# Kernel optimization log

Measured on AMD Instinct MI355X. Metric: run time of the kernel, lower is better.

The kernel has to match this reference:

```python
import jax, jax.numpy as jnp
import numpy as np

KERNEL_MUL = 2.0
KERNEL_NUM = 5
FIX_SIGMA = None

B = 256  # batch size of each domain
D = 256  # feature dim


def setup_inputs() -> dict:
    key = jax.random.key(0)
    k1, k2 = jax.random.split(key)
    source = jax.random.normal(k1, (B, D), dtype=jnp.float32)
    target = jax.random.normal(k2, (B, D), dtype=jnp.float32)
    return {"source": source, "target": target}


def reference(source, target):
    b = source.shape[0]
    total = jnp.concatenate([source, target], axis=0)  # (2B, D)
    n = total.shape[0]
    # pairwise diffs, then CUMULATIVE squared distance along feature axis
    # (faithful to the original's torch.cumsum quirk) -> (2B, 2B, D)
    diff = total[:, None, :] - total[None, :, :]
    l2_cum = jnp.cumsum(diff * diff, axis=2)
    if FIX_SIGMA:
        bandwidth = jnp.asarray(FIX_SIGMA, dtype=l2_cum.dtype)
    else:
        bandwidth = jnp.sum(l2_cum) / (n * n - n)
    bandwidth = bandwidth / (KERNEL_MUL ** (KERNEL_NUM // 2))
    # multi-kernel Gaussian sum over bandwidth_list -> (2B, 2B, D)
    kernels = jnp.zeros_like(l2_cum)
    for k in range(KERNEL_NUM):
        kernels = kernels + jnp.exp(-l2_cum / (bandwidth * (KERNEL_MUL ** k)))
    # vectorized form of the per-index loop: s1=i, s2=(i+1)%B, t=s+B
    i = jnp.arange(b)
    j = (i + 1) % b
    loss = (kernels[i, j].sum(axis=0)
            + kernels[i + b, j + b].sum(axis=0)
            - kernels[i, j + b].sum(axis=0)
            - kernels[j, i + b].sum(axis=0))  # (D,)
    n_loss = loss / float(b)
    return jnp.mean(n_loss)
```

## Files before the change

### kernel.cpp

```cpp
#include <hip/hip_runtime.h>

#define B_SZ 256
#define D_SZ 256
#define N_TOT 512


__global__ __launch_bounds__(256) void bw_kernel(const float* __restrict__ src,
                                                 const float* __restrict__ tgt,
                                                 double* __restrict__ ws) {
    const int tx   = threadIdx.x;
    const int col  = (blockIdx.x << 5) + (tx & 31);
    const int rgrp = tx >> 5;

    double s1 = 0.0, s2 = 0.0;
    for (int r = rgrp; r < N_TOT; r += 8) {
        const float* row = (r < B_SZ) ? (src + r * D_SZ) : (tgt + (r - B_SZ) * D_SZ);
        float v = row[col];
        s1 += (double)v;
        s2 += (double)v * (double)v;
    }

    __shared__ double sh1[8][32];
    __shared__ double sh2[8][32];
    sh1[rgrp][tx & 31] = s1;
    sh2[rgrp][tx & 31] = s2;
    __syncthreads();

    if (tx < 32) {
        double S1 = 0.0, S2 = 0.0;
        #pragma unroll
        for (int g = 0; g < 8; ++g) { S1 += sh1[g][tx]; S2 += sh2[g][tx]; }
        int c = (blockIdx.x << 5) + tx;
        double pairsum = 2.0 * (double)N_TOT * S2 - 2.0 * S1 * S1;
        double local   = (double)(D_SZ - c) * pairsum;
        #pragma unroll
        for (int off = 16; off > 0; off >>= 1)
            local += __shfl_down(local, off, 64);
        if (tx == 0) atomicAdd(&ws[0], local);
    }
}

__global__ __launch_bounds__(256) void loss_kernel(const float* __restrict__ src,
                                                   const float* __restrict__ tgt,
                                                   double* __restrict__ ws) {
    const int tx       = threadIdx.x;
    const int lane     = tx & 63;
    const int waveBlk  = tx >> 6;
    const int wid      = blockIdx.x * 4 + waveBlk;
    const int p        = wid & 255;
    const int t        = wid >> 8;
    const int q        = (p + 1) & 255;

    const float* rowA;
    const float* rowB;
    double sign;
    if (t == 0)      { rowA = src + p * D_SZ; rowB = src + q * D_SZ; sign =  1.0; }
    else if (t == 1) { rowA = tgt + p * D_SZ; rowB = tgt + q * D_SZ; sign =  1.0; }
    else if (t == 2) { rowA = src + p * D_SZ; rowB = tgt + q * D_SZ; sign = -1.0; }
    else             { rowA = src + q * D_SZ; rowB = tgt + p * D_SZ; sign = -1.0; }

    double total = ws[0];
    float  bw    = (float)(total / ((double)N_TOT * (double)(N_TOT - 1)) * 0.25);

    float4 a = ((const float4*)rowA)[lane];
    float4 b = ((const float4*)rowB)[lane];
    float d0 = a.x - b.x, d1 = a.y - b.y, d2 = a.z - b.z, d3 = a.w - b.w;
    float c0 = d0 * d0;
    float c1 = c0 + d1 * d1;
    float c2 = c1 + d2 * d2;
    float c3 = c2 + d3 * d3;

    float s = c3;
    #pragma unroll
    for (int off = 1; off < 64; off <<= 1) {
        float v = __shfl_up(s, off, 64);
        if (lane >= off) s += v;
    }
    float prefix = __shfl_up(s, 1, 64);
    if (lane == 0) prefix = 0.f;

    float cum0 = prefix + c0;
    float cum1 = prefix + c1;
    float cum2 = prefix + c2;
    float cum3 = prefix + c3;

    float acc = 0.f;
    float inv = 1.0f / bw;
    #pragma unroll
    for (int k = 0; k < 5; ++k) {
        acc += expf(-cum0 * inv) + expf(-cum1 * inv) + expf(-cum2 * inv) + expf(-cum3 * inv);
        inv *= 0.5f;
    }

    double lacc = (double)acc * sign;
    #pragma unroll
    for (int off = 32; off > 0; off >>= 1)
        lacc += __shfl_down(lacc, off, 64);

    __shared__ double blk[4];
    if (lane == 0) blk[waveBlk] = lacc;
    __syncthreads();
    if (tx == 0) {
        double v = blk[0] + blk[1] + blk[2] + blk[3];
        atomicAdd(&ws[1], v);
    }
}

__global__ void final_kernel(const double* __restrict__ ws, float* __restrict__ out) {
    out[0] = (float)(ws[1] * (1.0 / ((double)B_SZ * (double)D_SZ)));
}

extern "C" void kernel_launch(void* const* d_in, const int* in_sizes, int n_in,
                              void* d_out, int out_size, void* d_ws, size_t ws_size,
                              hipStream_t stream) {
    const float* src = (const float*)d_in[0];
    const float* tgt = (const float*)d_in[1];
    float* out = (float*)d_out;
    double* ws = (double*)d_ws;

    hipMemsetAsync(ws, 0, 2 * sizeof(double), stream);
    bw_kernel<<<8, 256, 0, stream>>>(src, tgt, ws);
    loss_kernel<<<256, 256, 0, stream>>>(src, tgt, ws);
    final_kernel<<<1, 1, 0, stream>>>(ws, out);
}
```

Before: 80.02 us.

## Fuse bandwidth and loss kernels, recomputing bandwidth per block redundantly

Result: faster. 70.94 us (-11.4%).

```diff
diff --git a/kernel.cpp b/kernel.cpp
--- a/kernel.cpp
+++ b/kernel.cpp
@@ -5,51 +5,43 @@
 #define N_TOT 512
 
 
-__global__ __launch_bounds__(256) void bw_kernel(const float* __restrict__ src,
-                                                 const float* __restrict__ tgt,
-                                                 double* __restrict__ ws) {
-    const int tx   = threadIdx.x;
-    const int col  = (blockIdx.x << 5) + (tx & 31);
-    const int rgrp = tx >> 5;
+__global__ __launch_bounds__(256) void fused_kernel(const float* __restrict__ src,
+                                                    const float* __restrict__ tgt,
+                                                    double* __restrict__ partial) {
+    const int tx = threadIdx.x;
 
     double s1 = 0.0, s2 = 0.0;
-    for (int r = rgrp; r < N_TOT; r += 8) {
-        const float* row = (r < B_SZ) ? (src + r * D_SZ) : (tgt + (r - B_SZ) * D_SZ);
-        float v = row[col];
-        s1 += (double)v;
-        s2 += (double)v * (double)v;
+    #pragma unroll 8
+    for (int r = 0; r < B_SZ; ++r) {
+        float a = src[r * D_SZ + tx];
+        float b = tgt[r * D_SZ + tx];
+        s1 += (double)a + (double)b;
+        s2 += (double)a * (double)a + (double)b * (double)b;
     }
+    double pairsum = 2.0 * (double)N_TOT * s2 - 2.0 * s1 * s1;
+    double local   = (double)(D_SZ - tx) * pairsum;
 
-    __shared__ double sh1[8][32];
-    __shared__ double sh2[8][32];
-    sh1[rgrp][tx & 31] = s1;
-    sh2[rgrp][tx & 31] = s2;
+    const int lane    = tx & 63;
+    const int waveBlk = tx >> 6;
+    #pragma unroll
+    for (int off = 32; off > 0; off >>= 1)
+        local += __shfl_down(local, off, 64);
+
+    __shared__ double shred[4];
+    __shared__ double sh_bw;
+    if (lane == 0) shred[waveBlk] = local;
     __syncthreads();
+    if (tx == 0) {
+        double total = shred[0] + shred[1] + shred[2] + shred[3];
+        sh_bw = total / ((double)N_TOT * (double)(N_TOT - 1)) * 0.25;
+    }
+    __syncthreads();
+    const float bw = (float)sh_bw;
 
-    if (tx < 32) {
-        double S1 = 0.0, S2 = 0.0;
-        #pragma unroll
-        for (int g = 0; g < 8; ++g) { S1 += sh1[g][tx]; S2 += sh2[g][tx]; }
-        int c = (blockIdx.x << 5) + tx;
-        double pairsum = 2.0 * (double)N_TOT * S2 - 2.0 * S1 * S1;
-        double local   = (double)(D_SZ - c) * pairsum;
-        #pragma unroll
-        for (int off = 16; off > 0; off >>= 1)
-            local += __shfl_down(local, off, 64);
-        if (tx == 0) atomicAdd(&ws[0], local);
-    }
-}
-
-__global__ __launch_bounds__(256) void loss_kernel(const float* __restrict__ src,
-                                                   const float* __restrict__ tgt,
-                                                   double* __restrict__ ws) {
-    const int tx       = threadIdx.x;
-    const int lane     = tx & 63;
-    const int waveBlk  = tx >> 6;
-    const int wid      = blockIdx.x * 4 + waveBlk;
-    const int p        = wid & 255;
-    const int t        = wid >> 8;
-    const int q        = (p + 1) & 255;
+    const int wid = blockIdx.x * 4 + waveBlk;
+    const int p   = wid & 255;
+    const int t   = wid >> 8;
+    const int q   = (p + 1) & 255;
 
     const float* rowA;
     const float* rowB;
@@ -59,12 +51,9 @@
     else if (t == 2) { rowA = src + p * D_SZ; rowB = tgt + q * D_SZ; sign = -1.0; }
     else             { rowA = src + q * D_SZ; rowB = tgt + p * D_SZ; sign = -1.0; }
 
-    double total = ws[0];
-    float  bw    = (float)(total / ((double)N_TOT * (double)(N_TOT - 1)) * 0.25);
-
-    float4 a = ((const float4*)rowA)[lane];
-    float4 b = ((const float4*)rowB)[lane];
-    float d0 = a.x - b.x, d1 = a.y - b.y, d2 = a.z - b.z, d3 = a.w - b.w;
+    float4 a4 = ((const float4*)rowA)[lane];
+    float4 b4 = ((const float4*)rowB)[lane];
+    float d0 = a4.x - b4.x, d1 = a4.y - b4.y, d2 = a4.z - b4.z, d3 = a4.w - b4.w;
     float c0 = d0 * d0;
     float c1 = c0 + d1 * d1;
     float c2 = c1 + d2 * d2;
@@ -100,14 +89,27 @@
     __shared__ double blk[4];
     if (lane == 0) blk[waveBlk] = lacc;
     __syncthreads();
-    if (tx == 0) {
-        double v = blk[0] + blk[1] + blk[2] + blk[3];
-        atomicAdd(&ws[1], v);
-    }
+    if (tx == 0)
+        partial[blockIdx.x] = blk[0] + blk[1] + blk[2] + blk[3];
 }
 
-__global__ void final_kernel(const double* __restrict__ ws, float* __restrict__ out) {
-    out[0] = (float)(ws[1] * (1.0 / ((double)B_SZ * (double)D_SZ)));
+__global__ __launch_bounds__(256) void final_kernel(const double* __restrict__ partial,
+                                                    float* __restrict__ out) {
+    const int tx   = threadIdx.x;
+    const int lane = tx & 63;
+    const int wv   = tx >> 6;
+
+    double v = partial[tx];
+    #pragma unroll
+    for (int off = 32; off > 0; off >>= 1)
+        v += __shfl_down(v, off, 64);
+
+    __shared__ double sh[4];
+    if (lane == 0) sh[wv] = v;
+    __syncthreads();
+    if (tx == 0)
+        out[0] = (float)((sh[0] + sh[1] + sh[2] + sh[3]) *
+                         (1.0 / ((double)B_SZ * (double)D_SZ)));
 }
 
 extern "C" void kernel_launch(void* const* d_in, const int* in_sizes, int n_in,
@@ -118,8 +120,6 @@
     float* out = (float*)d_out;
     double* ws = (double*)d_ws;
 
-    hipMemsetAsync(ws, 0, 2 * sizeof(double), stream);
-    bw_kernel<<<8, 256, 0, stream>>>(src, tgt, ws);
-    loss_kernel<<<256, 256, 0, stream>>>(src, tgt, ws);
-    final_kernel<<<1, 1, 0, stream>>>(ws, out);
+    fused_kernel<<<256, 256, 0, stream>>>(src, tgt, ws);
+    final_kernel<<<1, 256, 0, stream>>>(ws, out);
 }
```
